# Optimization experiments

Hardware: AMD Instinct MI355X
Metric: run time of the kernel (lower is better)

## Reference

```python
import jax, jax.numpy as jnp
import numpy as np

B, S, D, H = 8, 1024, 512, 8


def setup_inputs() -> dict:
    key = jax.random.key(0)
    ks = jax.random.split(key, 10)
    sc = 0.05
    return {
        "x": jax.random.normal(ks[0], (B, S, D), dtype=jnp.float32),
        "Wq": jax.random.normal(ks[1], (H, D, D), dtype=jnp.float32) * sc,
        "bq": jax.random.normal(ks[2], (H, D), dtype=jnp.float32) * sc,
        "Wk": jax.random.normal(ks[3], (H, D, D), dtype=jnp.float32) * sc,
        "bk": jax.random.normal(ks[4], (H, D), dtype=jnp.float32) * sc,
        "Wv": jax.random.normal(ks[5], (H, D, D), dtype=jnp.float32) * sc,
        "bv": jax.random.normal(ks[6], (H, D), dtype=jnp.float32) * sc,
        "Wo": jax.random.normal(ks[7], (H * D, D), dtype=jnp.float32) * sc,
        "bo": jax.random.normal(ks[8], (D,), dtype=jnp.float32) * sc,
    }


def reference(x, Wq, bq, Wk, bk, Wv, bv, Wo, bo):
    # Per-head full-dim projections, batched across heads.
    # x: [B,S,D]; Wq/Wk/Wv: [H,D,D]; b*: [H,D]
    q = jnp.einsum('bsd,hde->bhse', x, Wq) + bq[None, :, None, :]
    k = jnp.einsum('bsd,hde->bhse', x, Wk) + bk[None, :, None, :]
    v = jnp.einsum('bsd,hde->bhse', x, Wv) + bv[None, :, None, :]
    d = x.shape[-1]
    scores = jnp.einsum('bhse,bhte->bhst', q, k) / jnp.sqrt(jnp.float32(d))
    attn = jax.nn.softmax(scores, axis=-1)
    heads = jnp.einsum('bhst,bhte->bhse', attn, v)  # [B,H,S,D]
    # concat along feature dim (head order matches torch cat order)
    concat = jnp.transpose(heads, (0, 2, 1, 3)).reshape(x.shape[0], x.shape[1], -1)
    return concat @ Wo + bo
```

## Files before the change

kernel.cpp:

```cpp
#include <hip/hip_runtime.h>
#include <cstdint>
#include <cstddef>

#define BB 8
#define SS 1024
#define DDIM 512
#define HH 8
#define BS 8192
#define HD 4096

typedef __attribute__((ext_vector_type(4))) float f32x4;
typedef __attribute__((ext_vector_type(8))) short bf16x8;
typedef __attribute__((ext_vector_type(4))) unsigned short u16x4;


__device__ __forceinline__ unsigned short f2bf(float f) {
  union { float f; unsigned int u; } x; x.f = f;
  unsigned int r = x.u + 0x7fffu + ((x.u >> 16) & 1u);
  return (unsigned short)(r >> 16);
}

__device__ __forceinline__ void gload16(const void* g, void* l) {
  __builtin_amdgcn_global_load_lds(
      (const __attribute__((address_space(1))) unsigned int*)g,
      (__attribute__((address_space(3))) unsigned int*)l, 16, 0, 0);
}

#define BAR_LGKM() do { asm volatile("s_waitcnt lgkmcnt(0)" ::: "memory"); \
                        __builtin_amdgcn_s_barrier(); } while (0)
#define BAR_ALL()  do { asm volatile("s_waitcnt vmcnt(0) lgkmcnt(0)" ::: "memory"); \
                        __builtin_amdgcn_s_barrier(); } while (0)


__global__ void k_convert(const float* __restrict__ in, unsigned short* __restrict__ out, int n4) {
  int i = blockIdx.x * blockDim.x + threadIdx.x;
  if (i < n4) {
    float4 v = ((const float4*)in)[i];
    u16x4 o;
    o[0] = f2bf(v.x); o[1] = f2bf(v.y); o[2] = f2bf(v.z); o[3] = f2bf(v.w);
    ((u16x4*)out)[i] = o;
  }
}

__global__ void k_transpose_f2b(const float* __restrict__ in, unsigned short* __restrict__ out,
                                int R, int C) {
  __shared__ unsigned short tile[64][65];
  const int z = blockIdx.z;
  const int r0 = blockIdx.x << 6, c0 = blockIdx.y << 6;
  const float* ip = in + (size_t)z * R * C;
  unsigned short* op = out + (size_t)z * R * C;
  const int t = threadIdx.x;
#pragma unroll
  for (int i = 0; i < 16; ++i) {
    int idx = t + (i << 8); int r = idx >> 6, c = idx & 63;
    tile[r][c] = f2bf(ip[(size_t)(r0 + r) * C + (c0 + c)]);
  }
  __syncthreads();
#pragma unroll
  for (int i = 0; i < 16; ++i) {
    int idx = t + (i << 8); int c = idx >> 6, r = idx & 63;
    op[(size_t)(c0 + c) * R + (r0 + r)] = tile[r][c];
  }
}

template<int A_RS, int B_RS, int KITERS>
__device__ __forceinline__ void gemm_core(const char* Ag, const char* Bg,
                                          char* As, char* Bs, f32x4 acc[4][4]) {
  const int tid = threadIdx.x;
  const int wave = tid >> 6, lane = tid & 63;
  const int wr = (wave >> 1) << 6, wc = (wave & 1) << 6;
  const int srow = (wave << 3) + (lane >> 3);
  const int scol = ((lane & 7) << 4) ^ ((lane >> 3) << 4);

  for (int kb = 0; kb < KITERS; ++kb) {
    __syncthreads();
#pragma unroll
    for (int j = 0; j < 4; ++j) {
      gload16(Ag + (size_t)(j * 32 + srow) * A_RS + (size_t)kb * 128 + scol,
              As + j * 4096 + wave * 1024);
      gload16(Bg + (size_t)(j * 32 + srow) * B_RS + (size_t)kb * 128 + scol,
              Bs + j * 4096 + wave * 1024);
    }
    asm volatile("s_waitcnt vmcnt(0)" ::: "memory");
    __syncthreads();
#pragma unroll
    for (int ks = 0; ks < 2; ++ks) {
      bf16x8 af[4], bfr[4];
      const int kcol = (ks << 6) + ((lane >> 4) << 4);
#pragma unroll
      for (int i = 0; i < 4; ++i) {
        const int ar = wr + (i << 4) + (lane & 15);
        af[i] = *(const bf16x8*)(As + ar * 128 + (kcol ^ ((ar & 7) << 4)));
        const int br = wc + (i << 4) + (lane & 15);
        bfr[i] = *(const bf16x8*)(Bs + br * 128 + (kcol ^ ((br & 7) << 4)));
      }
#pragma unroll
      for (int i = 0; i < 4; ++i)
#pragma unroll
        for (int j = 0; j < 4; ++j)
          acc[i][j] = __builtin_amdgcn_mfma_f32_16x16x32_bf16(af[i], bfr[j], acc[i][j], 0, 0, 0);
    }
  }
}

__global__ __launch_bounds__(256, 2) void k_gemm_qkv(
    const unsigned short* __restrict__ xbf,
    const unsigned short* __restrict__ wqT, const unsigned short* __restrict__ wkT,
    const unsigned short* __restrict__ wvT,
    const float* __restrict__ bq, const float* __restrict__ bk, const float* __restrict__ bv,
    unsigned short* __restrict__ Qo, unsigned short* __restrict__ Ko,
    unsigned short* __restrict__ VTo, int b0) {
  __shared__ __align__(16) char As[16384], Bs[16384];
  const int idx = blockIdx.x;
  const int xcd = idx & 7;
  const int q = idx >> 3;
  const int m0 = (q & 15) << 7;
  const int zn = ((q >> 4) << 3) + xcd;
  const int z = zn >> 2;
  const int n0 = (zn & 3) << 7;
  const int p = z >> 3, h = z & 7;
  const unsigned short* wT = (p == 0) ? wqT : (p == 1) ? wkT : wvT;
  const float* bias = ((p == 0) ? bq : (p == 1) ? bk : bv) + (h << 9);
  const char* Ag = (const char*)xbf + ((size_t)(b0 << 10) + m0) * 1024;
  const char* Bg = (const char*)wT + (size_t)h * 524288 + (size_t)n0 * 1024;
  f32x4 acc[4][4] = {};
  gemm_core<1024, 1024, 8>(Ag, Bg, As, Bs, acc);

  const int tid = threadIdx.x, wave = tid >> 6, lane = tid & 63;
  const int wr = (wave >> 1) << 6, wc = (wave & 1) << 6;
  if (p == 2) {
#pragma unroll
    for (int j = 0; j < 4; ++j) {
      const int col = n0 + wc + (j << 4) + (lane & 15);
      const float bb = bias[col];
#pragma unroll
      for (int i = 0; i < 4; ++i) {
        const int sb = m0 + wr + (i << 4) + ((lane >> 4) << 2);
        const int lb = sb >> 10, s = sb & 1023;
        u16x4 o;
#pragma unroll
        for (int r = 0; r < 4; ++r) o[r] = f2bf(acc[i][j][r] + bb);
        *(u16x4*)(VTo + (size_t)(lb * HH + h) * 524288 +
                  (size_t)(((s >> 5) << 9) + col) * 32 + (s & 31)) = o;
      }
    }
  } else {
    unsigned short* dst = (p == 0) ? Qo : Ko;
#pragma unroll
    for (int j = 0; j < 4; ++j) {
      const int col = n0 + wc + (j << 4) + (lane & 15);
      const float bb = bias[col];
#pragma unroll
      for (int i = 0; i < 4; ++i)
#pragma unroll
        for (int r = 0; r < 4; ++r) {
          const int m = m0 + wr + (i << 4) + ((lane >> 4) << 2) + r;
          const int lb = m >> 10, s = m & 1023;
          dst[((size_t)((lb * HH + h) * SS + s) << 9) + col] = f2bf(acc[i][j][r] + bb);
        }
    }
  }
}

__global__ __launch_bounds__(256, 2) void k_gemm_out(
    const unsigned short* __restrict__ concat, const unsigned short* __restrict__ woT,
    const float* __restrict__ bo, float* __restrict__ out) {
  __shared__ __align__(16) char As[16384], Bs[16384];
  const int idx = blockIdx.x;
  const int xcd = idx & 7;
  const int n0 = (xcd & 3) << 7;
  const int m0 = ((idx >> 3) + ((xcd >> 2) << 5)) << 7;
  const char* Ag = (const char*)concat + (size_t)m0 * 8192;
  const char* Bg = (const char*)woT + (size_t)n0 * 8192;
  f32x4 acc[4][4] = {};
  gemm_core<8192, 8192, 64>(Ag, Bg, As, Bs, acc);

  const int tid = threadIdx.x, wave = tid >> 6, lane = tid & 63;
  const int wr = (wave >> 1) << 6, wc = (wave & 1) << 6;
#pragma unroll
  for (int j = 0; j < 4; ++j) {
    const int col = n0 + wc + (j << 4) + (lane & 15);
    const float bb = bo[col];
#pragma unroll
    for (int i = 0; i < 4; ++i)
#pragma unroll
      for (int r = 0; r < 4; ++r) {
        const int m = m0 + wr + (i << 4) + ((lane >> 4) << 2) + r;
        out[(size_t)m * DDIM + col] = acc[i][j][r] + bb;
      }
  }
}

__global__ __launch_bounds__(512, 1) void k_attn(
    const unsigned short* __restrict__ Qg, const unsigned short* __restrict__ Kg,
    const unsigned short* __restrict__ VT2g, unsigned short* __restrict__ Og,
    int b0) {
  __shared__ __align__(16) char smem[145408];
  float* Ssm = (float*)(smem + 131072);
  char*  Psm = smem + 139520;
  float* msm = (float*)(smem + 144640);
  float* lsm = (float*)(smem + 144896);
  float* fsm = (float*)(smem + 145152);

  const int tid = threadIdx.x, wave = tid >> 6, lane = tid & 63;
  const int bh = blockIdx.x & 15;
  const int qt = blockIdx.x >> 4;
  const int q0 = qt << 6;
  const char* Qb = (const char*)Qg + (size_t)bh * 1048576;
  const char* Kb = (const char*)Kg + (size_t)bh * 1048576;
  const char* Vb = (const char*)VT2g + (size_t)bh * 1048576;

  const int qi = wave >> 1, ni = wave & 1;
  const int l15 = lane & 15;
  const int kg16 = (lane >> 4) << 4;

  if (tid < 64) { msm[tid] = -1e30f; lsm[tid] = 0.0f; }

#define STAGE_K(KV0, BUF)                                                      \
  {                                                                            \
    _Pragma("unroll")                                                          \
    for (int j = 0; j < 4; ++j) {                                              \
      const int row = (j << 3) + wave;                                         \
      gload16(Kb + (size_t)((KV0) + row) * 1024 + ((lane << 4) ^ ((row & 7) << 4)), \
              smem + (BUF) * 32768 + row * 1024);                              \
    }                                                                          \
  }
#define STAGE_V(KT, BUF)                                                       \
  {                                                                            \
    const char* vsrc = Vb + (size_t)(KT) * 32768;                              \
    _Pragma("unroll")                                                          \
    for (int j = 0; j < 4; ++j) {                                              \
      const int idx = (j << 3) + wave;                                         \
      gload16(vsrc + idx * 1024 + (size_t)((lane >> 2) << 6) +                 \
                  ((((lane & 3) ^ ((lane >> 3) & 3))) << 4),                   \
              smem + 65536 + (BUF) * 32768 + idx * 1024);                      \
    }                                                                          \
  }

  bf16x8 qf[16];
  {
    const char* qrow = Qb + (size_t)(q0 + (qi << 4) + l15) * 1024 + kg16;
#pragma unroll
    for (int ks = 0; ks < 16; ++ks)
      qf[ks] = *(const bf16x8*)(qrow + (ks << 6));
  }
  STAGE_K(0, 0);
  STAGE_V(0, 0);

  f32x4 accO[4][4] = {};
  const float scale = 0.044194173824159216f;

  for (int kt = 0; kt < 32; ++kt) {
    const int cur = kt & 1;
    BAR_ALL();
    if (kt != 31) {
      STAGE_K((kt + 1) << 5, cur ^ 1);
      STAGE_V(kt + 1, cur ^ 1);
    }

    {
      f32x4 a0 = {}, a1 = {}, a2 = {}, a3 = {};
      const int krow = (ni << 4) + l15;
      const char* kb2 = smem + cur * 32768 + krow * 1024;
      const int ksz = (krow & 7) << 4;
      __builtin_amdgcn_s_setprio(1);
#pragma unroll
      for (int ks = 0; ks < 16; ks += 4) {
        const bf16x8 k0 = *(const bf16x8*)(kb2 + ((((ks + 0) << 6) + kg16) ^ ksz));
        const bf16x8 k1 = *(const bf16x8*)(kb2 + ((((ks + 1) << 6) + kg16) ^ ksz));
        const bf16x8 k2 = *(const bf16x8*)(kb2 + ((((ks + 2) << 6) + kg16) ^ ksz));
        const bf16x8 k3 = *(const bf16x8*)(kb2 + ((((ks + 3) << 6) + kg16) ^ ksz));
        a0 = __builtin_amdgcn_mfma_f32_16x16x32_bf16(qf[ks + 0], k0, a0, 0, 0, 0);
        a1 = __builtin_amdgcn_mfma_f32_16x16x32_bf16(qf[ks + 1], k1, a1, 0, 0, 0);
        a2 = __builtin_amdgcn_mfma_f32_16x16x32_bf16(qf[ks + 2], k2, a2, 0, 0, 0);
        a3 = __builtin_amdgcn_mfma_f32_16x16x32_bf16(qf[ks + 3], k3, a3, 0, 0, 0);
      }
      __builtin_amdgcn_s_setprio(0);
      const f32x4 s = (a0 + a1) + (a2 + a3);
      const int srow = (qi << 4) + ((lane >> 4) << 2);
      const int scol = (ni << 4) + l15;
#pragma unroll
      for (int r = 0; r < 4; ++r) Ssm[(srow + r) * 33 + scol] = s[r];
    }
    BAR_LGKM();

    {
      const int row = tid >> 3, c8 = tid & 7;
      float sv[4];
#pragma unroll
      for (int c = 0; c < 4; ++c) sv[c] = Ssm[row * 33 + (c8 << 2) + c] * scale;
      float mx = fmaxf(fmaxf(sv[0], sv[1]), fmaxf(sv[2], sv[3]));
      mx = fmaxf(mx, __shfl_xor(mx, 1));
      mx = fmaxf(mx, __shfl_xor(mx, 2));
      mx = fmaxf(mx, __shfl_xor(mx, 4));
      const float mold = msm[row];
      const float mnew = fmaxf(mold, mx);
      const float fac = __expf(mold - mnew);
      float ls = 0.0f;
      u16x4 pv;
#pragma unroll
      for (int c = 0; c < 4; ++c) {
        const float p = __expf(sv[c] - mnew);
        ls += p;
        pv[c] = f2bf(p);
      }
      ls += __shfl_xor(ls, 1);
      ls += __shfl_xor(ls, 2);
      ls += __shfl_xor(ls, 4);
      if ((tid & 7) == 0) {
        msm[row] = mnew;
        lsm[row] = lsm[row] * fac + ls;
        fsm[row] = fac;
      }
      *(u16x4*)(Psm + row * 80 + (c8 << 3)) = pv;
    }
    BAR_LGKM();

    {
      float facs[4][4];
      bf16x8 pf[4], vf[4];
      const int rb = (lane >> 4) << 2;
      const char* vb2 = smem + 65536 + cur * 32768;
      const int vswz = ((l15 >> 1) & 3) << 4;
#pragma unroll
      for (int i = 0; i < 4; ++i) {
#pragma unroll
        for (int r = 0; r < 4; ++r) facs[i][r] = fsm[(i << 4) + rb + r];
        pf[i] = *(const bf16x8*)(Psm + ((i << 4) + l15) * 80 + kg16);
      }
#pragma unroll
      for (int j = 0; j < 4; ++j) {
        const int vr = (wave << 6) + (j << 4) + l15;
        vf[j] = *(const bf16x8*)(vb2 + vr * 64 + (kg16 ^ vswz));
      }
#pragma unroll
      for (int i = 0; i < 4; ++i)
#pragma unroll
        for (int j = 0; j < 4; ++j)
#pragma unroll
          for (int r = 0; r < 4; ++r) accO[i][j][r] *= facs[i][r];
      __builtin_amdgcn_s_setprio(1);
#pragma unroll
      for (int i = 0; i < 4; ++i)
#pragma unroll
        for (int j = 0; j < 4; ++j)
          accO[i][j] = __builtin_amdgcn_mfma_f32_16x16x32_bf16(pf[i], vf[j], accO[i][j], 0, 0, 0);
      __builtin_amdgcn_s_setprio(0);
    }
  }

  {
    const int b = b0 + (bh >> 3), h = bh & 7;
    const int rb = (lane >> 4) << 2;
    float linv[4][4];
#pragma unroll
    for (int i = 0; i < 4; ++i)
#pragma unroll
      for (int r = 0; r < 4; ++r) linv[i][r] = 1.0f / lsm[(i << 4) + rb + r];
#pragma unroll
    for (int i = 0; i < 4; ++i)
#pragma unroll
      for (int j = 0; j < 4; ++j) {
        const int col = (wave << 6) + (j << 4) + l15;
#pragma unroll
        for (int r = 0; r < 4; ++r) {
          const int s = q0 + (i << 4) + rb + r;
          Og[((size_t)((b << 10) + s)) * HD + (h << 9) + col] = f2bf(accO[i][j][r] * linv[i][r]);
        }
      }
  }
#undef STAGE_K
#undef STAGE_V
}


extern "C" void kernel_launch(void* const* d_in, const int* in_sizes, int n_in,
                              void* d_out, int out_size, void* d_ws, size_t ws_size,
                              hipStream_t stream) {
  const float* x  = (const float*)d_in[0];
  const float* Wq = (const float*)d_in[1];
  const float* bq = (const float*)d_in[2];
  const float* Wk = (const float*)d_in[3];
  const float* bk = (const float*)d_in[4];
  const float* Wv = (const float*)d_in[5];
  const float* bv = (const float*)d_in[6];
  const float* Wo = (const float*)d_in[7];
  const float* bo = (const float*)d_in[8];
  float* out = (float*)d_out;
  char* ws = (char*)d_ws;

  unsigned short* xbf = (unsigned short*)(ws);
  unsigned short* wqT = (unsigned short*)(ws + 8388608);
  unsigned short* wkT = (unsigned short*)(ws + 12582912);
  unsigned short* wvT = (unsigned short*)(ws + 16777216);
  unsigned short* woT = (unsigned short*)(ws + 20971520);
  unsigned short* Cw  = (unsigned short*)(ws + 25165824);
  unsigned short* Qp  = (unsigned short*)(ws + 92274688);
  unsigned short* Kp  = (unsigned short*)(ws + 92274688 + 16777216ull);
  unsigned short* VTp = (unsigned short*)(ws + 92274688 + 2 * 16777216ull);

  k_convert<<<4096, 256, 0, stream>>>(x, xbf, BS * DDIM / 4);
  k_transpose_f2b<<<dim3(8, 8, 8), 256, 0, stream>>>(Wq, wqT, 512, 512);
  k_transpose_f2b<<<dim3(8, 8, 8), 256, 0, stream>>>(Wk, wkT, 512, 512);
  k_transpose_f2b<<<dim3(8, 8, 8), 256, 0, stream>>>(Wv, wvT, 512, 512);
  k_transpose_f2b<<<dim3(64, 8, 1), 256, 0, stream>>>(Wo, woT, 4096, 512);

  for (int b0 = 0; b0 < BB; b0 += 2) {
    k_gemm_qkv<<<dim3(1536), 256, 0, stream>>>(xbf, wqT, wkT, wvT,
                                               bq, bk, bv, Qp, Kp, VTp, b0);
    k_attn<<<dim3(256), 512, 0, stream>>>(Qp, Kp, VTp, Cw, b0);
  }

  k_gemm_out<<<dim3(256), 256, 0, stream>>>(Cw, woT, bo, out);
}
```

Before: 594.8 us.

## Process 64-key tiles per iteration with single-buffered K and register-prefetched V

The attention loop now handles 64 keys per iteration instead of 32, halving the number of iterations and barriers. Each wave computes two 16-row Q fragments against one K fragment, so each K load feeds two MFMAs. K is now single-buffered and reloaded after the scores are written. V is read into registers at the start of each iteration so the next V tiles can be staged early. This trades more LDS and registers for fewer barriers and softmax passes, with a risk of exposed K load latency because K is no longer double-buffered.

```diff
diff --git a/kernel.cpp b/kernel.cpp
--- a/kernel.cpp
+++ b/kernel.cpp
@@ -12,6 +12,7 @@
 typedef __attribute__((ext_vector_type(4))) float f32x4;
 typedef __attribute__((ext_vector_type(8))) short bf16x8;
 typedef __attribute__((ext_vector_type(4))) unsigned short u16x4;
+typedef __attribute__((ext_vector_type(8))) unsigned short u16x8;
 
 
 __device__ __forceinline__ unsigned short f2bf(float f) {
@@ -195,12 +196,12 @@
     const unsigned short* __restrict__ Qg, const unsigned short* __restrict__ Kg,
     const unsigned short* __restrict__ VT2g, unsigned short* __restrict__ Og,
     int b0) {
-  __shared__ __align__(16) char smem[145408];
+  __shared__ __align__(16) char smem[158464];
   float* Ssm = (float*)(smem + 131072);
-  char*  Psm = smem + 139520;
-  float* msm = (float*)(smem + 144640);
-  float* lsm = (float*)(smem + 144896);
-  float* fsm = (float*)(smem + 145152);
+  char*  Psm = smem + 148480;
+  float* msm = (float*)(smem + 157696);
+  float* lsm = (float*)(smem + 157952);
+  float* fsm = (float*)(smem + 158208);
 
   const int tid = threadIdx.x, wave = tid >> 6, lane = tid & 63;
   const int bh = blockIdx.x & 15;
@@ -210,86 +211,101 @@
   const char* Kb = (const char*)Kg + (size_t)bh * 1048576;
   const char* Vb = (const char*)VT2g + (size_t)bh * 1048576;
 
-  const int qi = wave >> 1, ni = wave & 1;
+  const int qi = wave >> 2, ni = wave & 3;
   const int l15 = lane & 15;
   const int kg16 = (lane >> 4) << 4;
 
   if (tid < 64) { msm[tid] = -1e30f; lsm[tid] = 0.0f; }
 
-#define STAGE_K(KV0, BUF)                                                      \
+#define STAGE_K(KV0)                                                           \
   {                                                                            \
     _Pragma("unroll")                                                          \
-    for (int j = 0; j < 4; ++j) {                                              \
+    for (int j = 0; j < 8; ++j) {                                              \
       const int row = (j << 3) + wave;                                         \
       gload16(Kb + (size_t)((KV0) + row) * 1024 + ((lane << 4) ^ ((row & 7) << 4)), \
-              smem + (BUF) * 32768 + row * 1024);                              \
+              smem + row * 1024);                                              \
     }                                                                          \
   }
-#define STAGE_V(KT, BUF)                                                       \
+#define STAGE_V(KT2, T)                                                        \
   {                                                                            \
-    const char* vsrc = Vb + (size_t)(KT) * 32768;                              \
+    const char* vsrc = Vb + (size_t)(KT2) * 32768;                             \
     _Pragma("unroll")                                                          \
     for (int j = 0; j < 4; ++j) {                                              \
       const int idx = (j << 3) + wave;                                         \
       gload16(vsrc + idx * 1024 + (size_t)((lane >> 2) << 6) +                 \
                   ((((lane & 3) ^ ((lane >> 3) & 3))) << 4),                   \
-              smem + 65536 + (BUF) * 32768 + idx * 1024);                      \
+              smem + 65536 + (T) * 32768 + idx * 1024);                        \
     }                                                                          \
   }
 
-  bf16x8 qf[16];
-  {
-    const char* qrow = Qb + (size_t)(q0 + (qi << 4) + l15) * 1024 + kg16;
+  bf16x8 qf[2][16];
+#pragma unroll
+  for (int f = 0; f < 2; ++f) {
+    const char* qrow = Qb + (size_t)(q0 + (qi << 5) + (f << 4) + l15) * 1024 + kg16;
 #pragma unroll
     for (int ks = 0; ks < 16; ++ks)
-      qf[ks] = *(const bf16x8*)(qrow + (ks << 6));
-  }
-  STAGE_K(0, 0);
+      qf[f][ks] = *(const bf16x8*)(qrow + (ks << 6));
+  }
+  STAGE_K(0);
   STAGE_V(0, 0);
+  STAGE_V(1, 1);
 
   f32x4 accO[4][4] = {};
   const float scale = 0.044194173824159216f;
-
-  for (int kt = 0; kt < 32; ++kt) {
-    const int cur = kt & 1;
+  const int vswz = ((l15 >> 1) & 3) << 4;
+
+  for (int kt = 0; kt < 16; ++kt) {
     BAR_ALL();
-    if (kt != 31) {
-      STAGE_K((kt + 1) << 5, cur ^ 1);
-      STAGE_V(kt + 1, cur ^ 1);
-    }
+
+    bf16x8 vf[2][4];
+#pragma unroll
+    for (int t = 0; t < 2; ++t)
+#pragma unroll
+      for (int j = 0; j < 4; ++j) {
+        const int vr = (wave << 6) + (j << 4) + l15;
+        vf[t][j] = *(const bf16x8*)(smem + 65536 + t * 32768 + vr * 64 + (kg16 ^ vswz));
+      }
+    BAR_LGKM();
+    if (kt != 15) { STAGE_V((kt << 1) + 2, 0); STAGE_V((kt << 1) + 3, 1); }
 
     {
-      f32x4 a0 = {}, a1 = {}, a2 = {}, a3 = {};
+      f32x4 a00 = {}, a01 = {}, a10 = {}, a11 = {};
       const int krow = (ni << 4) + l15;
-      const char* kb2 = smem + cur * 32768 + krow * 1024;
+      const char* kb2 = smem + krow * 1024;
       const int ksz = (krow & 7) << 4;
       __builtin_amdgcn_s_setprio(1);
 #pragma unroll
-      for (int ks = 0; ks < 16; ks += 4) {
-        const bf16x8 k0 = *(const bf16x8*)(kb2 + ((((ks + 0) << 6) + kg16) ^ ksz));
-        const bf16x8 k1 = *(const bf16x8*)(kb2 + ((((ks + 1) << 6) + kg16) ^ ksz));
-        const bf16x8 k2 = *(const bf16x8*)(kb2 + ((((ks + 2) << 6) + kg16) ^ ksz));
-        const bf16x8 k3 = *(const bf16x8*)(kb2 + ((((ks + 3) << 6) + kg16) ^ ksz));
-        a0 = __builtin_amdgcn_mfma_f32_16x16x32_bf16(qf[ks + 0], k0, a0, 0, 0, 0);
-        a1 = __builtin_amdgcn_mfma_f32_16x16x32_bf16(qf[ks + 1], k1, a1, 0, 0, 0);
-        a2 = __builtin_amdgcn_mfma_f32_16x16x32_bf16(qf[ks + 2], k2, a2, 0, 0, 0);
-        a3 = __builtin_amdgcn_mfma_f32_16x16x32_bf16(qf[ks + 3], k3, a3, 0, 0, 0);
+      for (int ks = 0; ks < 16; ks += 2) {
+        const bf16x8 kf0 = *(const bf16x8*)(kb2 + ((((ks + 0) << 6) + kg16) ^ ksz));
+        const bf16x8 kf1 = *(const bf16x8*)(kb2 + ((((ks + 1) << 6) + kg16) ^ ksz));
+        a00 = __builtin_amdgcn_mfma_f32_16x16x32_bf16(qf[0][ks + 0], kf0, a00, 0, 0, 0);
+        a10 = __builtin_amdgcn_mfma_f32_16x16x32_bf16(qf[1][ks + 0], kf0, a10, 0, 0, 0);
+        a01 = __builtin_amdgcn_mfma_f32_16x16x32_bf16(qf[0][ks + 1], kf1, a01, 0, 0, 0);
+        a11 = __builtin_amdgcn_mfma_f32_16x16x32_bf16(qf[1][ks + 1], kf1, a11, 0, 0, 0);
       }
       __builtin_amdgcn_s_setprio(0);
-      const f32x4 s = (a0 + a1) + (a2 + a3);
-      const int srow = (qi << 4) + ((lane >> 4) << 2);
+      const f32x4 s0 = a00 + a01;
+      const f32x4 s1 = a10 + a11;
+      const int srow = (qi << 5) + ((lane >> 4) << 2);
       const int scol = (ni << 4) + l15;
 #pragma unroll
-      for (int r = 0; r < 4; ++r) Ssm[(srow + r) * 33 + scol] = s[r];
+      for (int r = 0; r < 4; ++r) Ssm[(srow + r) * 68 + scol] = s0[r];
+#pragma unroll
+      for (int r = 0; r < 4; ++r) Ssm[(srow + 16 + r) * 68 + scol] = s1[r];
     }
     BAR_LGKM();
+    if (kt != 15) STAGE_K((kt + 1) << 6);
 
     {
       const int row = tid >> 3, c8 = tid & 7;
-      float sv[4];
-#pragma unroll
-      for (int c = 0; c < 4; ++c) sv[c] = Ssm[row * 33 + (c8 << 2) + c] * scale;
-      float mx = fmaxf(fmaxf(sv[0], sv[1]), fmaxf(sv[2], sv[3]));
+      f32x4 sv0 = *(const f32x4*)(Ssm + row * 68 + (c8 << 3));
+      f32x4 sv1 = *(const f32x4*)(Ssm + row * 68 + (c8 << 3) + 4);
+      float mx = -1e30f;
+#pragma unroll
+      for (int c = 0; c < 4; ++c) {
+        sv0[c] *= scale; sv1[c] *= scale;
+        mx = fmaxf(mx, fmaxf(sv0[c], sv1[c]));
+      }
       mx = fmaxf(mx, __shfl_xor(mx, 1));
       mx = fmaxf(mx, __shfl_xor(mx, 2));
       mx = fmaxf(mx, __shfl_xor(mx, 4));
@@ -297,12 +313,14 @@
       const float mnew = fmaxf(mold, mx);
       const float fac = __expf(mold - mnew);
       float ls = 0.0f;
-      u16x4 pv;
+      u16x8 pv;
 #pragma unroll
       for (int c = 0; c < 4; ++c) {
-        const float p = __expf(sv[c] - mnew);
-        ls += p;
-        pv[c] = f2bf(p);
+        const float p0 = __expf(sv0[c] - mnew);
+        const float p1 = __expf(sv1[c] - mnew);
+        ls += p0 + p1;
+        pv[c] = f2bf(p0);
+        pv[c + 4] = f2bf(p1);
       }
       ls += __shfl_xor(ls, 1);
       ls += __shfl_xor(ls, 2);
@@ -312,39 +330,33 @@
         lsm[row] = lsm[row] * fac + ls;
         fsm[row] = fac;
       }
-      *(u16x4*)(Psm + row * 80 + (c8 << 3)) = pv;
+      *(u16x8*)(Psm + row * 144 + (c8 << 4)) = pv;
     }
     BAR_LGKM();
 
     {
-      float facs[4][4];
-      bf16x8 pf[4], vf[4];
       const int rb = (lane >> 4) << 2;
-      const char* vb2 = smem + 65536 + cur * 32768;
-      const int vswz = ((l15 >> 1) & 3) << 4;
 #pragma unroll
       for (int i = 0; i < 4; ++i) {
-#pragma unroll
-        for (int r = 0; r < 4; ++r) facs[i][r] = fsm[(i << 4) + rb + r];
-        pf[i] = *(const bf16x8*)(Psm + ((i << 4) + l15) * 80 + kg16);
-      }
-#pragma unroll
-      for (int j = 0; j < 4; ++j) {
-        const int vr = (wave << 6) + (j << 4) + l15;
-        vf[j] = *(const bf16x8*)(vb2 + vr * 64 + (kg16 ^ vswz));
-      }
-#pragma unroll
-      for (int i = 0; i < 4; ++i)
+        const f32x4 fv = *(const f32x4*)(fsm + (i << 4) + rb);
 #pragma unroll
         for (int j = 0; j < 4; ++j)
 #pragma unroll
-          for (int r = 0; r < 4; ++r) accO[i][j][r] *= facs[i][r];
+          for (int r = 0; r < 4; ++r) accO[i][j][r] *= fv[r];
+      }
       __builtin_amdgcn_s_setprio(1);
 #pragma unroll
-      for (int i = 0; i < 4; ++i)
-#pragma unroll
-        for (int j = 0; j < 4; ++j)
-          accO[i][j] = __builtin_amdgcn_mfma_f32_16x16x32_bf16(pf[i], vf[j], accO[i][j], 0, 0, 0);
+      for (int t = 0; t < 2; ++t) {
+        bf16x8 pf[4];
+#pragma unroll
+        for (int i = 0; i < 4; ++i)
+          pf[i] = *(const bf16x8*)(Psm + ((i << 4) + l15) * 144 + (t << 6) + kg16);
+#pragma unroll
+        for (int i = 0; i < 4; ++i)
+#pragma unroll
+          for (int j = 0; j < 4; ++j)
+            accO[i][j] = __builtin_amdgcn_mfma_f32_16x16x32_bf16(pf[i], vf[t][j], accO[i][j], 0, 0, 0);
+      }
       __builtin_amdgcn_s_setprio(0);
     }
   }
```

New measurement: 1.005 ms. +68.9%, slower.
